# Kernel optimization log

Measured on AMD Instinct MI355X. Metric: run time of the kernel, lower is better.

The kernel has to match this reference:

```python
import jax, jax.numpy as jnp
import numpy as np

BATCH, SEQ_LEN, INPUT_DIM, HIDDEN, OUT_DIM = 4096, 2048, 5, 64, 1
DT = 0.1


def setup_inputs() -> dict:
    key = jax.random.key(0)
    ks = jax.random.split(key, 8)
    return {
        "x": jax.random.normal(ks[0], (BATCH, SEQ_LEN, INPUT_DIM), dtype=jnp.float32),
        # torch.rand(hidden)*0.5 + 0.1  -> uniform in [0.1, 0.6)
        "time_constants": jax.random.uniform(ks[1], (HIDDEN,), dtype=jnp.float32) * 0.5 + 0.1,
        "W_ih_w": jax.random.normal(ks[2], (HIDDEN, INPUT_DIM), dtype=jnp.float32) * (1.0 / np.sqrt(INPUT_DIM)),
        "W_ih_b": jax.random.normal(ks[3], (HIDDEN,), dtype=jnp.float32) * 0.02,
        "W_hh_w": jax.random.normal(ks[4], (HIDDEN, HIDDEN), dtype=jnp.float32) * (1.0 / np.sqrt(HIDDEN)),
        "W_hh_b": jax.random.normal(ks[5], (HIDDEN,), dtype=jnp.float32) * 0.02,
        "out_w": jax.random.normal(ks[6], (OUT_DIM, HIDDEN), dtype=jnp.float32) * (1.0 / np.sqrt(HIDDEN)),
        "out_b": jax.random.normal(ks[7], (OUT_DIM,), dtype=jnp.float32) * 0.02,
    }


def reference(x, time_constants, W_ih_w, W_ih_b, W_hh_w, W_hh_b, out_w, out_b):
    # x: [B, T, D_in]. Liquid-time-constant RNN: sequential scan over T.
    batch = x.shape[0]
    hidden = time_constants.shape[0]
    inv_tau = 1.0 / jnp.abs(time_constants)  # [H], hoisted out of the loop

    def step(h, x_t):
        # x_t: [B, D_in], h: [B, H]
        input_current = x_t @ W_ih_w.T + W_ih_b            # [B, H]
        recurrent_current = jnp.tanh(h) @ W_hh_w.T + W_hh_b  # [B, H]
        dhdt = -h * inv_tau + input_current + recurrent_current
        return h + DT * dhdt, None

    h0 = jnp.zeros((batch, hidden), dtype=x.dtype)
    xs = jnp.swapaxes(x, 0, 1)  # [T, B, D_in]
    h_final, _ = jax.lax.scan(step, h0, xs)
    return jnp.tanh(h_final) @ out_w.T + out_b  # [B, out_dim]
```

## Files before the change

### kernel.cpp

```cpp
#include <hip/hip_runtime.h>
#include <hip/hip_bf16.h>
#include <stdint.h>

#define SEQ     2048
#define DIN     5
#define HID     64
#define DTC     0.1f
#define BTILE   16
#define NWAVE   4
#define KSTR    72

typedef __attribute__((ext_vector_type(8))) __bf16  bf16x8;
typedef __attribute__((ext_vector_type(8))) short   short8;
typedef __attribute__((ext_vector_type(4))) float   f32x4;
typedef __attribute__((ext_vector_type(4))) int     i32x4;

__device__ __forceinline__ unsigned short f2bf(float f) {
    unsigned int u = __builtin_bit_cast(unsigned int, f);
    unsigned int r = (u + 0x7FFFu + ((u >> 16) & 1u)) >> 16;
    return (unsigned short)r;
}

__device__ __forceinline__ float fast_tanh(float x) {
    float e = __expf(2.0f * x);
    return 1.0f - 2.0f * __builtin_amdgcn_rcpf(e + 1.0f);
}

__device__ __forceinline__ unsigned int cvt_pk_bf16(float lo, float hi) {
    unsigned int r;
    asm("v_cvt_pk_bf16_f32 %0, %1, %2" : "=v"(r) : "v"(lo), "v"(hi));
    return r;
}

__global__ __launch_bounds__(256) void ltc_kernel(
    const float* __restrict__ x,
    const float* __restrict__ tau,
    const float* __restrict__ Wih,
    const float* __restrict__ bih,
    const float* __restrict__ Whh,
    const float* __restrict__ bhh,
    const float* __restrict__ outw,
    const float* __restrict__ outb,
    float* __restrict__ out)
{
    const int tid  = threadIdx.x;
    const int wave = tid >> 6;
    const int lane = tid & 63;
    const int lg   = lane >> 4;
    const int ln   = lane & 15;
    const int b0   = blockIdx.x * BTILE;

    __shared__ __align__(16) unsigned short tbuf[2][BTILE][KSTR];
    __shared__ float redbuf[NWAVE][4][BTILE];

    const int jbase = 16 * wave + 4 * lg;
    const int arow  = 16 * wave + ln;

    float a[4], ow[4];
#pragma unroll
    for (int r = 0; r < 4; ++r) {
        a[r]  = 1.0f - DTC / fabsf(tau[jbase + r]);
        ow[r] = outw[jbase + r];
    }

    short8 s0 = {0,0,0,0,0,0,0,0}, s1 = {0,0,0,0,0,0,0,0}, s2 = {0,0,0,0,0,0,0,0};
#pragma unroll
    for (int q = 0; q < 8; ++q) {
        s0[q] = (short)f2bf(DTC * Whh[arow * HID + lg * 8 + q]);
        s1[q] = (short)f2bf(DTC * Whh[arow * HID + 32 + lg * 8 + q]);
    }
    if (lg == 0) {
#pragma unroll
        for (int d = 0; d < DIN; ++d) s2[d] = (short)f2bf(DTC * Wih[arow * DIN + d]);
        s2[5] = (short)f2bf(DTC * (bih[arow] + bhh[arow]));
    }
    const bf16x8 Ahh0 = __builtin_bit_cast(bf16x8, s0);
    const bf16x8 Ahh1 = __builtin_bit_cast(bf16x8, s1);
    const bf16x8 Aix  = __builtin_bit_cast(bf16x8, s2);

    for (int i = tid; i < BTILE * KSTR; i += 256) (&tbuf[1][0][0])[i] = 0;

    const float* xp = x + (size_t)(b0 + ln) * (SEQ * DIN);
    float px0 = 0.f, px1 = 0.f, px2 = 0.f, px3 = 0.f, px4 = 0.f;
    if (lg == 0) { px0 = xp[0]; px1 = xp[1]; px2 = xp[2]; px3 = xp[3]; px4 = xp[4]; }

    f32x4 h = {0.f, 0.f, 0.f, 0.f};

    for (int t = 0; t < SEQ; ++t) {
        __syncthreads();

        const unsigned short* tb = &tbuf[(t + 1) & 1][0][0];
        i32x4 r0 = *(const i32x4*)(tb + ln * KSTR + lg * 8);
        i32x4 r1 = *(const i32x4*)(tb + ln * KSTR + 32 + lg * 8);

        short8 bxs = {0,0,0,0,0,0,0,0};
        if (lg == 0) {
            bxs[0] = (short)f2bf(px0); bxs[1] = (short)f2bf(px1);
            bxs[2] = (short)f2bf(px2); bxs[3] = (short)f2bf(px3);
            bxs[4] = (short)f2bf(px4); bxs[5] = (short)0x3F80;
            if (t + 1 < SEQ) {
                const float* xn = xp + (size_t)(t + 1) * DIN;
                px0 = xn[0]; px1 = xn[1]; px2 = xn[2]; px3 = xn[3]; px4 = xn[4];
            }
        }

        f32x4 c;
#pragma unroll
        for (int r = 0; r < 4; ++r) c[r] = a[r] * h[r];

        c = __builtin_amdgcn_mfma_f32_16x16x32_bf16(Aix,  __builtin_bit_cast(bf16x8, bxs), c, 0, 0, 0);
        c = __builtin_amdgcn_mfma_f32_16x16x32_bf16(Ahh0, __builtin_bit_cast(bf16x8, r0),  c, 0, 0, 0);
        c = __builtin_amdgcn_mfma_f32_16x16x32_bf16(Ahh1, __builtin_bit_cast(bf16x8, r1),  c, 0, 0, 0);
        h = c;

        float t0 = fast_tanh(h[0]);
        float t1 = fast_tanh(h[1]);
        float t2 = fast_tanh(h[2]);
        float t3 = fast_tanh(h[3]);
        unsigned long long w01 =
            ((unsigned long long)cvt_pk_bf16(t2, t3) << 32) | (unsigned long long)cvt_pk_bf16(t0, t1);
        *(unsigned long long*)(&tbuf[t & 1][0][0] + ln * KSTR + jbase) = w01;
    }

    float part = fast_tanh(h[0]) * ow[0] + fast_tanh(h[1]) * ow[1]
               + fast_tanh(h[2]) * ow[2] + fast_tanh(h[3]) * ow[3];
    redbuf[wave][lg][ln] = part;
    __syncthreads();
    if (tid < BTILE) {
        float s = outb[0];
#pragma unroll
        for (int w = 0; w < NWAVE; ++w)
#pragma unroll
            for (int g = 0; g < 4; ++g) s += redbuf[w][g][tid];
        out[b0 + tid] = s;
    }
}

extern "C" void kernel_launch(void* const* d_in, const int* in_sizes, int n_in,
                              void* d_out, int out_size, void* d_ws, size_t ws_size,
                              hipStream_t stream) {
    const float* x    = (const float*)d_in[0];
    const float* tau  = (const float*)d_in[1];
    const float* Wih  = (const float*)d_in[2];
    const float* bih  = (const float*)d_in[3];
    const float* Whh  = (const float*)d_in[4];
    const float* bhh  = (const float*)d_in[5];
    const float* outw = (const float*)d_in[6];
    const float* outb = (const float*)d_in[7];
    float* out = (float*)d_out;

    const int batch = in_sizes[0] / (SEQ * DIN);
    ltc_kernel<<<batch / BTILE, NWAVE * 64, 0, stream>>>(x, tau, Wih, bih, Whh, bhh, outw, outb, out);
}
```

Before: 552.0 us.

## Swizzle LDS tanh buffer for linear reads, unroll by two, prefetch x two steps ahead

Replaces the padded [16][72] LDS tile with a layout that puts each MFMA B-operand fragment at lane*16 bytes, so every step reads two contiguous 16-byte chunks per lane and needs no per-step address math. The time loop is unrolled by two with fixed ping-pong buffer pointers, and x is prefetched two steps ahead in registers. The x operand is packed with the hardware bf16 convert and masked instead of using a per-lane branch. These cut per-step VALU and address work and LDS bank conflicts on the serial critical path, at the cost of more registers and a less obvious layout.

```diff
diff --git a/kernel.cpp b/kernel.cpp
--- a/kernel.cpp
+++ b/kernel.cpp
@@ -8,17 +8,16 @@
 #define DTC     0.1f
 #define BTILE   16
 #define NWAVE   4
-#define KSTR    72
 
 typedef __attribute__((ext_vector_type(8))) __bf16  bf16x8;
 typedef __attribute__((ext_vector_type(8))) short   short8;
 typedef __attribute__((ext_vector_type(4))) float   f32x4;
 typedef __attribute__((ext_vector_type(4))) int     i32x4;
+typedef unsigned long long u64;
 
 __device__ __forceinline__ unsigned short f2bf(float f) {
     unsigned int u = __builtin_bit_cast(unsigned int, f);
-    unsigned int r = (u + 0x7FFFu + ((u >> 16) & 1u)) >> 16;
-    return (unsigned short)r;
+    return (unsigned short)((u + 0x7FFFu + ((u >> 16) & 1u)) >> 16);
 }
 
 __device__ __forceinline__ float fast_tanh(float x) {
@@ -50,7 +49,7 @@
     const int ln   = lane & 15;
     const int b0   = blockIdx.x * BTILE;
 
-    __shared__ __align__(16) unsigned short tbuf[2][BTILE][KSTR];
+    __shared__ __align__(16) unsigned short sbuf[2][1024];
     __shared__ float redbuf[NWAVE][4][BTILE];
 
     const int jbase = 16 * wave + 4 * lg;
@@ -78,49 +77,56 @@
     const bf16x8 Ahh1 = __builtin_bit_cast(bf16x8, s1);
     const bf16x8 Aix  = __builtin_bit_cast(bf16x8, s2);
 
-    for (int i = tid; i < BTILE * KSTR; i += 256) (&tbuf[1][0][0])[i] = 0;
+    const int wbyte = ((jbase >= 32) ? 1024 : 0) + (((jbase & 31) >> 3) * 256)
+                    + ln * 16 + (((jbase >> 2) & 1) * 8);
+    char* const wp0 = (char*)sbuf[0] + wbyte;
+    char* const wp1 = (char*)sbuf[1] + wbyte;
+    const char* const rp0 = (const char*)sbuf[0] + lane * 16;
+    const char* const rp1 = (const char*)sbuf[1] + lane * 16;
 
-    const float* xp = x + (size_t)(b0 + ln) * (SEQ * DIN);
-    float px0 = 0.f, px1 = 0.f, px2 = 0.f, px3 = 0.f, px4 = 0.f;
-    if (lg == 0) { px0 = xp[0]; px1 = xp[1]; px2 = xp[2]; px3 = xp[3]; px4 = xp[4]; }
+    ((u64*)sbuf[1])[tid] = 0ULL;
+
+    const unsigned int lmask = (lg == 0) ? 0xFFFFFFFFu : 0u;
+
+    const float* xb = x + (size_t)(b0 + ln) * (SEQ * DIN);
+    float eA0 = xb[0], eA1 = xb[1], eA2 = xb[2], eA3 = xb[3], eA4 = xb[4];
+    float oA0 = xb[5], oA1 = xb[6], oA2 = xb[7], oA3 = xb[8], oA4 = xb[9];
+    const float* xnext = xb + 2 * DIN;
 
     f32x4 h = {0.f, 0.f, 0.f, 0.f};
 
-    for (int t = 0; t < SEQ; ++t) {
-        __syncthreads();
+#define STEP(PAR, P0, P1, P2, P3, P4, PF, XOFF)                                    \
+    {                                                                              \
+        __syncthreads();                                                           \
+        const char* rb = (PAR) ? rp0 : rp1;                \
+        i32x4 r0 = *(const i32x4*)(rb);                                            \
+        i32x4 r1 = *(const i32x4*)(rb + 1024);                                     \
+        unsigned int bu0 = cvt_pk_bf16(P0, P1) & lmask;                            \
+        unsigned int bu1 = cvt_pk_bf16(P2, P3) & lmask;                            \
+        unsigned int bu2 = cvt_pk_bf16(P4, 1.0f) & lmask;                          \
+        i32x4 bx = { (int)bu0, (int)bu1, (int)bu2, 0 };                            \
+        if (PF) { P0 = xnext[(XOFF)+0]; P1 = xnext[(XOFF)+1]; P2 = xnext[(XOFF)+2];\
+                  P3 = xnext[(XOFF)+3]; P4 = xnext[(XOFF)+4]; }                    \
+        f32x4 c;                                                                   \
+        c[0] = a[0]*h[0]; c[1] = a[1]*h[1]; c[2] = a[2]*h[2]; c[3] = a[3]*h[3];    \
+        c = __builtin_amdgcn_mfma_f32_16x16x32_bf16(Aix,  __builtin_bit_cast(bf16x8, bx), c, 0, 0, 0); \
+        c = __builtin_amdgcn_mfma_f32_16x16x32_bf16(Ahh0, __builtin_bit_cast(bf16x8, r0), c, 0, 0, 0); \
+        c = __builtin_amdgcn_mfma_f32_16x16x32_bf16(Ahh1, __builtin_bit_cast(bf16x8, r1), c, 0, 0, 0); \
+        h = c;                                                                     \
+        float t0 = fast_tanh(h[0]), t1 = fast_tanh(h[1]);                          \
+        float t2 = fast_tanh(h[2]), t3 = fast_tanh(h[3]);                          \
+        u64 w01 = ((u64)cvt_pk_bf16(t2, t3) << 32) | (u64)cvt_pk_bf16(t0, t1);     \
+        *(u64*)((PAR) ? wp1 : wp0) = w01;                                          \
+    }
 
-        const unsigned short* tb = &tbuf[(t + 1) & 1][0][0];
-        i32x4 r0 = *(const i32x4*)(tb + ln * KSTR + lg * 8);
-        i32x4 r1 = *(const i32x4*)(tb + ln * KSTR + 32 + lg * 8);
-
-        short8 bxs = {0,0,0,0,0,0,0,0};
-        if (lg == 0) {
-            bxs[0] = (short)f2bf(px0); bxs[1] = (short)f2bf(px1);
-            bxs[2] = (short)f2bf(px2); bxs[3] = (short)f2bf(px3);
-            bxs[4] = (short)f2bf(px4); bxs[5] = (short)0x3F80;
-            if (t + 1 < SEQ) {
-                const float* xn = xp + (size_t)(t + 1) * DIN;
-                px0 = xn[0]; px1 = xn[1]; px2 = xn[2]; px3 = xn[3]; px4 = xn[4];
-            }
-        }
-
-        f32x4 c;
-#pragma unroll
-        for (int r = 0; r < 4; ++r) c[r] = a[r] * h[r];
-
-        c = __builtin_amdgcn_mfma_f32_16x16x32_bf16(Aix,  __builtin_bit_cast(bf16x8, bxs), c, 0, 0, 0);
-        c = __builtin_amdgcn_mfma_f32_16x16x32_bf16(Ahh0, __builtin_bit_cast(bf16x8, r0),  c, 0, 0, 0);
-        c = __builtin_amdgcn_mfma_f32_16x16x32_bf16(Ahh1, __builtin_bit_cast(bf16x8, r1),  c, 0, 0, 0);
-        h = c;
-
-        float t0 = fast_tanh(h[0]);
-        float t1 = fast_tanh(h[1]);
-        float t2 = fast_tanh(h[2]);
-        float t3 = fast_tanh(h[3]);
-        unsigned long long w01 =
-            ((unsigned long long)cvt_pk_bf16(t2, t3) << 32) | (unsigned long long)cvt_pk_bf16(t0, t1);
-        *(unsigned long long*)(&tbuf[t & 1][0][0] + ln * KSTR + jbase) = w01;
+    for (int t = 0; t < SEQ - 2; t += 2) {
+        STEP(0, eA0, eA1, eA2, eA3, eA4, true, 0)
+        STEP(1, oA0, oA1, oA2, oA3, oA4, true, DIN)
+        xnext += 2 * DIN;
     }
+    STEP(0, eA0, eA1, eA2, eA3, eA4, false, 0)
+    STEP(1, oA0, oA1, oA2, oA3, oA4, false, 0)
+#undef STEP
 
     float part = fast_tanh(h[0]) * ow[0] + fast_tanh(h[1]) * ow[1]
                + fast_tanh(h[2]) * ow[2] + fast_tanh(h[3]) * ow[3];
```

New measurement: 523.9 us. 5.1% less time.
